# Performance work log

Measured on AMD Instinct MI355X. Metric: run time of the kernel, lower is better.

## Reference

```python
import jax, jax.numpy as jnp
import numpy as np

D_MODEL = 96
D_STATE = 6
D_CONV = 9
D_INNER = 2 * D_MODEL          # expand = 2
DT_RANK = (D_MODEL + 15) // 16  # ceil(d_model/16) = 6
DIM_IN = 64
DIM_OUT = 64
BATCH = 16
SEQLEN = 4096


def setup_inputs() -> dict:
    key = jax.random.key(0)
    ks = jax.random.split(key, 12)
    def s(k, shape, scale=0.02):
        return jax.random.normal(k, shape, jnp.float32) * scale
    return {
        "x": jax.random.normal(ks[0], (BATCH, SEQLEN, D_MODEL), jnp.float32),
        # Mamba block params
        "in_proj_w": s(ks[1], (2 * D_INNER, D_MODEL)),
        "conv_w": s(ks[2], (D_INNER, D_CONV), 0.1),   # depthwise conv kernel
        "conv_b": jnp.zeros((D_INNER,), jnp.float32),
        "x_proj_w": s(ks[3], (DT_RANK + 2 * D_STATE, D_INNER)),
        "dt_proj_w": s(ks[4], (D_INNER, DT_RANK), 0.1),
        "dt_proj_b": s(ks[5], (D_INNER,), 0.1),
        "A_log": jnp.log(jnp.tile(jnp.arange(1, D_STATE + 1, dtype=jnp.float32), (D_INNER, 1))),
        "D_param": jnp.ones((D_INNER,), jnp.float32),
        "out_proj_w": s(ks[6], (D_MODEL, D_INNER)),
        "norm_w": jnp.ones((D_MODEL,), jnp.float32),  # RMSNorm weight
        # heads
        "out_fc_w": s(ks[7], (DIM_IN, D_MODEL)),
        "out_fc_b": jnp.zeros((DIM_IN,), jnp.float32),
        "mu_w": s(ks[8], (DIM_OUT, DIM_IN)),
        "mu_b": jnp.zeros((DIM_OUT,), jnp.float32),
        "sigma_w": s(ks[9], (DIM_OUT, DIM_IN)),
        "sigma_b": jnp.zeros((DIM_OUT,), jnp.float32),
    }


def _mamba_block(x, in_proj_w, conv_w, conv_b, x_proj_w, dt_proj_w, dt_proj_b,
                 A_log, D_param, out_proj_w):
    Bsz = x.shape[0]
    xz = jnp.einsum('bld,ed->ble', x, in_proj_w)          # (B,L,2*ED)
    xs, z = jnp.split(xz, 2, axis=-1)
    # causal depthwise conv1d (torch pads d_conv-1 both sides then trims right)
    xt = xs.transpose(0, 2, 1)                            # (B,ED,L)
    kern = conv_w[:, None, :]                             # (ED,1,K)
    xc = jax.lax.conv_general_dilated(xt, kern, window_strides=(1,),
                                      padding=[(D_CONV - 1, 0)],
                                      feature_group_count=D_INNER)
    xc = (xc + conv_b[None, :, None]).transpose(0, 2, 1)  # (B,L,ED)
    xc = jax.nn.silu(xc)
    dbc = jnp.einsum('ble,fe->blf', xc, x_proj_w)         # (B,L,dt_rank+2N)
    delta_r = dbc[..., :DT_RANK]
    Bm = dbc[..., DT_RANK:DT_RANK + D_STATE]              # (B,L,N)
    Cm = dbc[..., DT_RANK + D_STATE:]                     # (B,L,N)
    delta = jax.nn.softplus(jnp.einsum('blr,er->ble', delta_r, dt_proj_w) + dt_proj_b)
    A = -jnp.exp(A_log)                                   # (ED,N)
    deltaA = jnp.exp(delta[..., None] * A)                # (B,L,ED,N)
    BX = (delta * xc)[..., None] * Bm[:, :, None, :]      # (B,L,ED,N)

    def step(h, inputs):
        dA, bx = inputs
        h = dA * h + bx
        return h, h

    h0 = jnp.zeros((Bsz, D_INNER, D_STATE), x.dtype)
    _, hs = jax.lax.scan(step, h0, (deltaA.swapaxes(0, 1), BX.swapaxes(0, 1)))
    y = jnp.einsum('lben,bln->ble', hs, Cm)               # (B,L,ED)
    y = y + D_param * xc
    y = y * jax.nn.silu(z)
    return jnp.einsum('ble,de->bld', y, out_proj_w)       # (B,L,D)


def reference(x, in_proj_w, conv_w, conv_b, x_proj_w, dt_proj_w, dt_proj_b,
              A_log, D_param, out_proj_w, norm_w,
              out_fc_w, out_fc_b, mu_w, mu_b, sigma_w, sigma_b):
    # residual block: x + mixer(RMSNorm(x))   (dropout is identity at eval)
    h = x * jax.lax.rsqrt(jnp.mean(x * x, axis=-1, keepdims=True) + 1e-5) * norm_w
    out = x + _mamba_block(h, in_proj_w, conv_w, conv_b, x_proj_w,
                           dt_proj_w, dt_proj_b, A_log, D_param, out_proj_w)
    e = out.mean(axis=1)                                  # (B,D)
    feat = jax.nn.elu(jnp.tanh(e @ out_fc_w.T + out_fc_b))
    mu = feat @ mu_w.T + mu_b
    sigma = jax.nn.elu(feat @ sigma_w.T + sigma_b) + 1.0 + 1e-14
    return (feat, mu, sigma)
```

## Files before the change

### kernel.cpp

```cpp
#include <hip/hip_runtime.h>
#include <math.h>

#define BATCH 16
#define SEQLEN 4096
#define D_MODEL 96
#define D_STATE 6
#define D_CONV 9
#define D_INNER 192
#define DT_RANK 6
#define NPOS (BATCH * SEQLEN)

#define NC2 128
#define CT2 (SEQLEN / NC2)
#define NSEG 16
#define CPS (NC2 / NSEG)

#define OFF_XS    0L
#define OFF_Z     (OFF_XS   + (long)NPOS * 96)
#define OFF_OUT4  (OFF_Z    + (long)NPOS * 96)
#define OFF_SEG   (OFF_OUT4 + (long)BATCH * NC2 * 5 * 192 * 4)
#define OFF_XPART (OFF_SEG  + (long)BATCH * NSEG * 5 * 192 * 4)

typedef short v8s __attribute__((ext_vector_type(8)));
typedef float v4f __attribute__((ext_vector_type(4)));

__device__ __forceinline__ float silu_fast(float v) {
    return __fdividef(v, 1.0f + __expf(-v));
}
__device__ __forceinline__ float softplus_fast(float v) {
    return (v > 20.0f) ? v : __logf(1.0f + __expf(v));
}
__device__ __forceinline__ float eluf(float v) {
    return (v > 0.0f) ? v : expm1f(v);
}
__device__ __forceinline__ unsigned int pack_bf16(float a, float b) {
    unsigned int ua = __float_as_uint(a), ub = __float_as_uint(b);
    ua += 0x7FFFu + ((ua >> 16) & 1u);
    ub += 0x7FFFu + ((ub >> 16) & 1u);
    return (ua >> 16) | (ub & 0xFFFF0000u);
}
__device__ __forceinline__ unsigned short bf16h(float v) {
    unsigned int u = __float_as_uint(v);
    u += 0x7FFFu + ((u >> 16) & 1u);
    return (unsigned short)(u >> 16);
}
__device__ __forceinline__ float bf2f(unsigned short h) {
    return __uint_as_float(((unsigned int)h) << 16);
}

#define TP1 64
__global__ __launch_bounds__(256, 2) void k1_rmsnorm_inproj(
    const float* __restrict__ x, const float* __restrict__ W,
    const float* __restrict__ norm_w,
    unsigned short* __restrict__ xs, unsigned short* __restrict__ z,
    float* __restrict__ xpart)
{
    __shared__ unsigned int s_ovl[7680];
    __shared__ unsigned int s_hA[64 * 52];
    __shared__ float s_part[TP1][4];
    __shared__ float s_scale[TP1];
    float* hRow = (float*)s_ovl;
    unsigned int* WB = s_ovl;

    const int tid = threadIdx.x;
    const long p0 = (long)blockIdx.x * TP1;

    {
        const float4* x4 = (const float4*)&x[p0 * 96];
        for (int i = tid; i < TP1 * 24; i += 256) {
            int p = i / 24, dq = i - p * 24;
            float4 v = x4[i];
            float* hr = &hRow[p * 101 + dq * 4];
            hr[0] = v.x; hr[1] = v.y; hr[2] = v.z; hr[3] = v.w;
        }
    }
    __syncthreads();

    {
        int p = tid >> 2, g = tid & 3;
        float ss = 0.0f;
        for (int d = g; d < 96; d += 4) { float v = hRow[p * 101 + d]; ss += v * v; }
        s_part[p][g] = ss;
    }
    __syncthreads();

    if (tid < TP1) {
        float ss = s_part[tid][0] + s_part[tid][1] + s_part[tid][2] + s_part[tid][3];
        s_scale[tid] = 1.0f / sqrtf(ss / 96.0f + 1e-5f);
    } else if (tid < TP1 + 96) {
        int d = tid - TP1;
        float s = 0.0f;
        for (int p = 0; p < TP1; p++) s += hRow[p * 101 + d];
        xpart[(long)blockIdx.x * 96 + d] = s;
    }
    __syncthreads();

    {
        const float2* nw2 = (const float2*)norm_w;
        for (int i = tid; i < TP1 * 48; i += 256) {
            int p = i / 48, dp = i - p * 48;
            float sc = s_scale[p];
            float2 nv = nw2[dp];
            float v0 = hRow[p * 101 + 2 * dp]     * sc * nv.x;
            float v1 = hRow[p * 101 + 2 * dp + 1] * sc * nv.y;
            s_hA[p * 52 + dp] = pack_bf16(v0, v1);
        }
    }
    __syncthreads();

    const int wave = tid >> 6, lane = tid & 63;
    const int quad = lane >> 4, ln = lane & 15;
    const int n0 = wave * 96;
    unsigned int* WBw = WB + wave * 1920;

    v4f acc[4][6];
#pragma unroll
    for (int mt = 0; mt < 4; mt++)
#pragma unroll
        for (int nt = 0; nt < 6; nt++) acc[mt][nt] = (v4f){0.f, 0.f, 0.f, 0.f};

    for (int kc = 0; kc < 3; kc++) {
#pragma unroll 8
        for (int ii = 0; ii < 24; ii++) {
            int i = lane + ii * 64;
            int jp = i >> 4, kp = i & 15;
            const float2 wv = *(const float2*)&W[(n0 + jp) * 96 + kc * 32 + 2 * kp];
            WBw[jp * 20 + kp] = pack_bf16(wv.x, wv.y);
        }
        v8s bfh[4];
#pragma unroll
        for (int mt = 0; mt < 4; mt++)
            bfh[mt] = *(const v8s*)&s_hA[(mt * 16 + ln) * 52 + kc * 16 + quad * 4];
#pragma unroll
        for (int nt = 0; nt < 6; nt++) {
            v8s aw = *(const v8s*)&WBw[(nt * 16 + ln) * 20 + quad * 4];
#pragma unroll
            for (int mt = 0; mt < 4; mt++)
                acc[mt][nt] = __builtin_amdgcn_mfma_f32_16x16x32_bf16(
                    aw, bfh[mt], acc[mt][nt], 0, 0, 0);
        }
    }

    unsigned short* dst = (wave < 2) ? xs : z;
    const int jb = (wave & 1) * 96;
#pragma unroll
    for (int mt = 0; mt < 4; mt++) {
        long pos = p0 + mt * 16 + ln;
#pragma unroll
        for (int nt = 0; nt < 6; nt++) {
            uint2 v;
            v.x = pack_bf16(acc[mt][nt][0], acc[mt][nt][1]);
            v.y = pack_bf16(acc[mt][nt][2], acc[mt][nt][3]);
            *(uint2*)&dst[pos * D_INNER + jb + nt * 16 + quad * 4] = v;
        }
    }
}

#define SXSTR 200
__global__ __launch_bounds__(192, 4) void k2f_conv_scan(
    const unsigned short* __restrict__ xs, const unsigned short* __restrict__ z,
    const float* __restrict__ conv_w, const float* __restrict__ conv_b,
    const float* __restrict__ x_proj_w,
    const float* __restrict__ dt_w, const float* __restrict__ dt_b,
    const float* __restrict__ A_log, const float* __restrict__ D_param,
    float4* __restrict__ out4)
{
    __shared__ unsigned short sxc[CT2 * SXSTR];
    __shared__ unsigned short sxpB[18 * SXSTR];
    __shared__ float sMeta[CT2][20];
    const int e = threadIdx.x;
    const int c = blockIdx.x & (NC2 - 1);
    const int b = blockIdx.x >> 7;
    const int l0 = c * CT2;
    const long brow = (long)b * SEQLEN;

    {
        unsigned int* xpB = (unsigned int*)sxpB;
        for (int i = e; i < 18 * 96; i += 192) {
            int f = i / 96, kp = i - f * 96;
            const float2 wv = *(const float2*)&x_proj_w[f * 192 + 2 * kp];
            xpB[f * 100 + kp] = pack_bf16(wv.x, wv.y);
        }
    }

    float cw[D_CONV];
#pragma unroll
    for (int k = 0; k < D_CONV; k++) cw[k] = conv_w[e * D_CONV + k];
    const float cb = conv_b[e];
    float win[D_CONV];
#pragma unroll
    for (int k = 0; k < 8; k++) {
        int ll = l0 - 8 + k;
        win[k] = (ll >= 0) ? bf2f(xs[(brow + ll) * D_INNER + e]) : 0.0f;
    }
#pragma unroll
    for (int r = 0; r < CT2; r++) {
        win[8] = bf2f(xs[(brow + l0 + r) * D_INNER + e]);
        float s = cb;
#pragma unroll
        for (int k = 0; k < D_CONV; k++) s += win[k] * cw[k];
        sxc[r * SXSTR + e] = bf16h(silu_fast(s));
#pragma unroll
        for (int k = 0; k < 8; k++) win[k] = win[k + 1];
    }

    const unsigned short* zp = &z[(brow + l0) * D_INNER + e];
    float zv[CT2];
#pragma unroll
    for (int t = 0; t < CT2; t++) zv[t] = bf2f(zp[(long)t * D_INNER]);
    __syncthreads();

    {
        const int wave = e >> 6, lane = e & 63;
        const int quad = lane >> 4, ln = lane & 15;
        if (wave < 2) {
            const int mt = wave;
            const int r1 = (ln < 2) ? 16 + ln : 0;
            v4f dacc[2];
            dacc[0] = (v4f){0.f, 0.f, 0.f, 0.f};
            dacc[1] = (v4f){0.f, 0.f, 0.f, 0.f};
#pragma unroll
            for (int kc = 0; kc < 6; kc++) {
                v8s af  = *(const v8s*)&sxc[(mt * 16 + ln) * SXSTR + kc * 32 + quad * 8];
                v8s bf0 = *(const v8s*)&sxpB[ln * SXSTR + kc * 32 + quad * 8];
                v8s bf1 = *(const v8s*)&sxpB[r1 * SXSTR + kc * 32 + quad * 8];
                dacc[0] = __builtin_amdgcn_mfma_f32_16x16x32_bf16(af, bf0, dacc[0], 0, 0, 0);
                dacc[1] = __builtin_amdgcn_mfma_f32_16x16x32_bf16(af, bf1, dacc[1], 0, 0, 0);
            }
#pragma unroll
            for (int nt = 0; nt < 2; nt++) {
                int f = nt * 16 + ln;
                if (f < 18) {
                    int col = (f < 6) ? f : f + 2;
#pragma unroll
                    for (int r = 0; r < 4; r++)
                        sMeta[mt * 16 + quad * 4 + r][col] = dacc[nt][r];
                }
            }
        }
    }
    __syncthreads();

    float a[D_STATE];
#pragma unroll
    for (int n = 0; n < D_STATE; n++) a[n] = -__expf(A_log[e * D_STATE + n]);
    float dtw[DT_RANK];
#pragma unroll
    for (int q = 0; q < DT_RANK; q++) dtw[q] = dt_w[e * DT_RANK + q];
    const float dtb = dt_b[e];
    const float Dv = D_param[e];
    const float a0 = a[0];

    bool pok = true;
#pragma unroll
    for (int n = 1; n < D_STATE; n++)
        pok = pok && (fabsf(a[n] - (float)(n + 1) * a0)
                      <= 1e-4f * (float)(n + 1) * fabsf(a0));
    unsigned long long pmask = __ballot(pok);

    float S[D_STATE], G[D_STATE];
#pragma unroll
    for (int n = 0; n < D_STATE; n++) { S[n] = 0.0f; G[n] = 0.0f; }
    float ysum0 = 0.0f;

    if (pmask == 0xFFFFFFFFFFFFFFFFull) {
        float Pa = 1.0f;
#pragma unroll 2
        for (int t = 0; t < CT2; t++) {
            const float4* m4 = (const float4*)&sMeta[t][0];
            float4 m0 = m4[0], m1 = m4[1], mB0 = m4[2], mB1 = m4[3], mC = m4[4];
            float Bv[6] = {mB0.x, mB0.y, mB0.z, mB0.w, mB1.x, mB1.y};
            float Cv[6] = {mB1.z, mB1.w, mC.x, mC.y, mC.z, mC.w};
            float dr = dtb + m0.x * dtw[0] + m0.y * dtw[1] + m0.z * dtw[2]
                     + m0.w * dtw[3] + m1.x * dtw[4] + m1.y * dtw[5];
            float dl = softplus_fast(dr);
            float xv = bf2f(sxc[t * SXSTR + e]);
            float zw = silu_fast(zv[t]);
            float dx = dl * xv;
            float y = Dv * xv;
            float E = __expf(dl * a0);
            Pa *= E;
            float dA = E, Pn = Pa;
#pragma unroll
            for (int n = 0; n < D_STATE; n++) {
                S[n] = dA * S[n] + dx * Bv[n];
                y += S[n] * Cv[n];
                G[n] += zw * Pn * Cv[n];
                dA *= E;
                Pn *= Pa;
            }
            ysum0 += zw * y;
        }
        long ob = (long)(b * NC2 + c) * 5 * 192 + e;
        float P1 = Pa, P2 = P1 * Pa, P3 = P2 * Pa, P4 = P3 * Pa, P5 = P4 * Pa, P6 = P5 * Pa;
        float4 q0, q1, q2, q3, q4;
        q0.x=P1; q0.y=P2; q0.z=P3; q0.w=P4;
        q1.x=P5; q1.y=P6; q1.z=S[0]; q1.w=S[1];
        q2.x=S[2]; q2.y=S[3]; q2.z=S[4]; q2.w=S[5];
        q3.x=G[0]; q3.y=G[1]; q3.z=G[2]; q3.w=G[3];
        q4.x=G[4]; q4.y=G[5]; q4.z=ysum0; q4.w=0.0f;
        out4[ob          ] = q0;
        out4[ob + 192    ] = q1;
        out4[ob + 2 * 192] = q2;
        out4[ob + 3 * 192] = q3;
        out4[ob + 4 * 192] = q4;
    } else {
        float P[D_STATE];
#pragma unroll
        for (int n = 0; n < D_STATE; n++) P[n] = 1.0f;
#pragma unroll 2
        for (int t = 0; t < CT2; t++) {
            const float4* m4 = (const float4*)&sMeta[t][0];
            float4 m0 = m4[0], m1 = m4[1], mB0 = m4[2], mB1 = m4[3], mC = m4[4];
            float Bv[6] = {mB0.x, mB0.y, mB0.z, mB0.w, mB1.x, mB1.y};
            float Cv[6] = {mB1.z, mB1.w, mC.x, mC.y, mC.z, mC.w};
            float dr = dtb + m0.x * dtw[0] + m0.y * dtw[1] + m0.z * dtw[2]
                     + m0.w * dtw[3] + m1.x * dtw[4] + m1.y * dtw[5];
            float dl = softplus_fast(dr);
            float xv = bf2f(sxc[t * SXSTR + e]);
            float zw = silu_fast(zv[t]);
            float dx = dl * xv;
            float y = Dv * xv;
#pragma unroll
            for (int n = 0; n < D_STATE; n++) {
                float dA = __expf(dl * a[n]);
                S[n] = dA * S[n] + dx * Bv[n];
                P[n] *= dA;
                y += S[n] * Cv[n];
                G[n] += zw * P[n] * Cv[n];
            }
            ysum0 += zw * y;
        }
        long ob = (long)(b * NC2 + c) * 5 * 192 + e;
        float4 q0, q1, q2, q3, q4;
        q0.x=P[0]; q0.y=P[1]; q0.z=P[2]; q0.w=P[3];
        q1.x=P[4]; q1.y=P[5]; q1.z=S[0]; q1.w=S[1];
        q2.x=S[2]; q2.y=S[3]; q2.z=S[4]; q2.w=S[5];
        q3.x=G[0]; q3.y=G[1]; q3.z=G[2]; q3.w=G[3];
        q4.x=G[4]; q4.y=G[5]; q4.z=ysum0; q4.w=0.0f;
        out4[ob          ] = q0;
        out4[ob + 192    ] = q1;
        out4[ob + 2 * 192] = q2;
        out4[ob + 3 * 192] = q3;
        out4[ob + 4 * 192] = q4;
    }
}

__global__ __launch_bounds__(192) void k4_seg(
    const float4* __restrict__ out4, float4* __restrict__ seg4)
{
    const int e = threadIdx.x;
    const int s = blockIdx.x & (NSEG - 1);
    const int b = blockIdx.x >> 4;

    float H[D_STATE], Gq[D_STATE], Pp[D_STATE];
#pragma unroll
    for (int n = 0; n < D_STATE; n++) { H[n] = 0.0f; Gq[n] = 0.0f; Pp[n] = 1.0f; }
    float yb = 0.0f;
#pragma unroll 2
    for (int cc = 0; cc < CPS; cc++) {
        int c = s * CPS + cc;
        long ob = (long)(b * NC2 + c) * 5 * 192 + e;
        float4 q0 = out4[ob];
        float4 q1 = out4[ob + 192];
        float4 q2 = out4[ob + 2 * 192];
        float4 q3 = out4[ob + 3 * 192];
        float4 q4 = out4[ob + 4 * 192];
        float Pv[6] = {q0.x, q0.y, q0.z, q0.w, q1.x, q1.y};
        float Sv[6] = {q1.z, q1.w, q2.x, q2.y, q2.z, q2.w};
        float Gv[6] = {q3.x, q3.y, q3.z, q3.w, q4.x, q4.y};
        float g = 0.0f;
#pragma unroll
        for (int n = 0; n < D_STATE; n++) g += Gv[n] * H[n];
        yb += q4.z + g;
#pragma unroll
        for (int n = 0; n < D_STATE; n++) {
            Gq[n] += Gv[n] * Pp[n];
            H[n] = Pv[n] * H[n] + Sv[n];
            Pp[n] *= Pv[n];
        }
    }
    long sb = (long)(b * NSEG + s) * 5 * 192 + e;
    float4 q0, q1, q2, q3, q4;
    q0.x=Pp[0]; q0.y=Pp[1]; q0.z=Pp[2]; q0.w=Pp[3];
    q1.x=Pp[4]; q1.y=Pp[5]; q1.z=H[0]; q1.w=H[1];
    q2.x=H[2]; q2.y=H[3]; q2.z=H[4]; q2.w=H[5];
    q3.x=Gq[0]; q3.y=Gq[1]; q3.z=Gq[2]; q3.w=Gq[3];
    q4.x=Gq[4]; q4.y=Gq[5]; q4.z=yb; q4.w=0.0f;
    seg4[sb          ] = q0;
    seg4[sb + 192    ] = q1;
    seg4[sb + 2 * 192] = q2;
    seg4[sb + 3 * 192] = q3;
    seg4[sb + 4 * 192] = q4;
}

__global__ __launch_bounds__(192) void k4_head(
    const float4* __restrict__ seg4, const float* __restrict__ xpart,
    const float* __restrict__ Wout,
    const float* __restrict__ fc_w, const float* __restrict__ fc_b,
    const float* __restrict__ mu_w, const float* __restrict__ mu_b,
    const float* __restrict__ sg_w, const float* __restrict__ sg_b,
    float* __restrict__ out)
{
    __shared__ float ybar[D_INNER];
    __shared__ float sxb[D_MODEL];
    __shared__ float evec[D_MODEL];
    __shared__ float feat_s[64];
    const int e = threadIdx.x;
    const int b = blockIdx.x;

    float H[D_STATE];
#pragma unroll
    for (int n = 0; n < D_STATE; n++) H[n] = 0.0f;
    float yb = 0.0f;
#pragma unroll 4
    for (int s = 0; s < NSEG; s++) {
        long ob = (long)(b * NSEG + s) * 5 * 192 + e;
        float4 q0 = seg4[ob];
        float4 q1 = seg4[ob + 192];
        float4 q2 = seg4[ob + 2 * 192];
        float4 q3 = seg4[ob + 3 * 192];
        float4 q4 = seg4[ob + 4 * 192];
        float Pv[6] = {q0.x, q0.y, q0.z, q0.w, q1.x, q1.y};
        float Sv[6] = {q1.z, q1.w, q2.x, q2.y, q2.z, q2.w};
        float Gv[6] = {q3.x, q3.y, q3.z, q3.w, q4.x, q4.y};
        float g = 0.0f;
#pragma unroll
        for (int n = 0; n < D_STATE; n++) g += Gv[n] * H[n];
        yb += q4.z + g;
#pragma unroll
        for (int n = 0; n < D_STATE; n++) H[n] = Pv[n] * H[n] + Sv[n];
    }
    ybar[e] = yb;

    if (e < D_MODEL) {
        const float* xp = &xpart[(long)b * 64 * 96 + e];
        float s = 0.0f;
        for (int t = 0; t < 64; t++) s += xp[t * 96];
        sxb[e] = s;
    }
    __syncthreads();

    if (e < D_MODEL) {
        float s = sxb[e];
        const float* wrow = &Wout[e * D_INNER];
        for (int e2 = 0; e2 < D_INNER; e2++) s += ybar[e2] * wrow[e2];
        evec[e] = s / (float)SEQLEN;
    }
    __syncthreads();

    if (e < 64) {
        float s = fc_b[e];
        const float* wrow = &fc_w[e * D_MODEL];
        for (int d = 0; d < D_MODEL; d++) s += evec[d] * wrow[d];
        float f = eluf(tanhf(s));
        feat_s[e] = f;
        out[b * 64 + e] = f;
    }
    __syncthreads();

    if (e < 64) {
        float smu = mu_b[e], ssg = sg_b[e];
        const float* mrow = &mu_w[e * 64];
        const float* srow = &sg_w[e * 64];
        for (int i = 0; i < 64; i++) {
            smu += feat_s[i] * mrow[i];
            ssg += feat_s[i] * srow[i];
        }
        out[1024 + b * 64 + e] = smu;
        out[2048 + b * 64 + e] = eluf(ssg) + 1.0f + 1e-14f;
    }
}

extern "C" void kernel_launch(void* const* d_in, const int* in_sizes, int n_in,
                              void* d_out, int out_size, void* d_ws, size_t ws_size,
                              hipStream_t stream) {
    const float* x         = (const float*)d_in[0];
    const float* in_proj_w = (const float*)d_in[1];
    const float* conv_w    = (const float*)d_in[2];
    const float* conv_b    = (const float*)d_in[3];
    const float* x_proj_w  = (const float*)d_in[4];
    const float* dt_proj_w = (const float*)d_in[5];
    const float* dt_proj_b = (const float*)d_in[6];
    const float* A_log     = (const float*)d_in[7];
    const float* D_param   = (const float*)d_in[8];
    const float* out_proj_w= (const float*)d_in[9];
    const float* norm_w    = (const float*)d_in[10];
    const float* out_fc_w  = (const float*)d_in[11];
    const float* out_fc_b  = (const float*)d_in[12];
    const float* mu_w      = (const float*)d_in[13];
    const float* mu_b      = (const float*)d_in[14];
    const float* sigma_w   = (const float*)d_in[15];
    const float* sigma_b   = (const float*)d_in[16];
    float* ws = (float*)d_ws;
    float* out = (float*)d_out;

    k1_rmsnorm_inproj<<<NPOS / TP1, 256, 0, stream>>>(
        x, in_proj_w, norm_w,
        (unsigned short*)(ws + OFF_XS), (unsigned short*)(ws + OFF_Z),
        ws + OFF_XPART);

    k2f_conv_scan<<<BATCH * NC2, 192, 0, stream>>>(
        (const unsigned short*)(ws + OFF_XS), (const unsigned short*)(ws + OFF_Z),
        conv_w, conv_b, x_proj_w,
        dt_proj_w, dt_proj_b, A_log, D_param,
        (float4*)(ws + OFF_OUT4));

    k4_seg<<<BATCH * NSEG, 192, 0, stream>>>(
        (const float4*)(ws + OFF_OUT4), (float4*)(ws + OFF_SEG));

    k4_head<<<BATCH, 192, 0, stream>>>(
        (const float4*)(ws + OFF_SEG), ws + OFF_XPART, out_proj_w,
        out_fc_w, out_fc_b, mu_w, mu_b, sigma_w, sigma_b, out);
}
```

Baseline: 202.1 us.

## Halve scan chunk count to 64 per batch, doubling chunk length

The conv+scan kernel now uses 64 chunks of 64 timesteps instead of 128 chunks of 32. This halves the number of blocks and per-chunk summaries written and later combined, and each chunk's MFMA x_proj now covers four 16-row tiles. The z values are loaded in two 32-step batches to keep register pressure bounded. Fewer blocks (1024) means less parallelism and a longer serial recurrence per thread, and shared memory per block doubles, which may lower occupancy.

```diff
diff --git a/kernel.cpp b/kernel.cpp
--- a/kernel.cpp
+++ b/kernel.cpp
@@ -10,7 +10,7 @@
 #define DT_RANK 6
 #define NPOS (BATCH * SEQLEN)
 
-#define NC2 128
+#define NC2 64
 #define CT2 (SEQLEN / NC2)
 #define NSEG 16
 #define CPS (NC2 / NSEG)
@@ -170,7 +170,7 @@
     __shared__ float sMeta[CT2][20];
     const int e = threadIdx.x;
     const int c = blockIdx.x & (NC2 - 1);
-    const int b = blockIdx.x >> 7;
+    const int b = blockIdx.x >> 6;
     const int l0 = c * CT2;
     const long brow = (long)b * SEQLEN;
 
@@ -203,38 +203,36 @@
 #pragma unroll
         for (int k = 0; k < 8; k++) win[k] = win[k + 1];
     }
-
-    const unsigned short* zp = &z[(brow + l0) * D_INNER + e];
-    float zv[CT2];
-#pragma unroll
-    for (int t = 0; t < CT2; t++) zv[t] = bf2f(zp[(long)t * D_INNER]);
     __syncthreads();
 
     {
         const int wave = e >> 6, lane = e & 63;
         const int quad = lane >> 4, ln = lane & 15;
         if (wave < 2) {
-            const int mt = wave;
             const int r1 = (ln < 2) ? 16 + ln : 0;
-            v4f dacc[2];
-            dacc[0] = (v4f){0.f, 0.f, 0.f, 0.f};
-            dacc[1] = (v4f){0.f, 0.f, 0.f, 0.f};
-#pragma unroll
-            for (int kc = 0; kc < 6; kc++) {
-                v8s af  = *(const v8s*)&sxc[(mt * 16 + ln) * SXSTR + kc * 32 + quad * 8];
-                v8s bf0 = *(const v8s*)&sxpB[ln * SXSTR + kc * 32 + quad * 8];
-                v8s bf1 = *(const v8s*)&sxpB[r1 * SXSTR + kc * 32 + quad * 8];
-                dacc[0] = __builtin_amdgcn_mfma_f32_16x16x32_bf16(af, bf0, dacc[0], 0, 0, 0);
-                dacc[1] = __builtin_amdgcn_mfma_f32_16x16x32_bf16(af, bf1, dacc[1], 0, 0, 0);
-            }
-#pragma unroll
-            for (int nt = 0; nt < 2; nt++) {
-                int f = nt * 16 + ln;
-                if (f < 18) {
-                    int col = (f < 6) ? f : f + 2;
-#pragma unroll
-                    for (int r = 0; r < 4; r++)
-                        sMeta[mt * 16 + quad * 4 + r][col] = dacc[nt][r];
+#pragma unroll
+            for (int half = 0; half < 2; half++) {
+                const int mt = wave * 2 + half;
+                v4f dacc[2];
+                dacc[0] = (v4f){0.f, 0.f, 0.f, 0.f};
+                dacc[1] = (v4f){0.f, 0.f, 0.f, 0.f};
+#pragma unroll
+                for (int kc = 0; kc < 6; kc++) {
+                    v8s af  = *(const v8s*)&sxc[(mt * 16 + ln) * SXSTR + kc * 32 + quad * 8];
+                    v8s bf0 = *(const v8s*)&sxpB[ln * SXSTR + kc * 32 + quad * 8];
+                    v8s bf1 = *(const v8s*)&sxpB[r1 * SXSTR + kc * 32 + quad * 8];
+                    dacc[0] = __builtin_amdgcn_mfma_f32_16x16x32_bf16(af, bf0, dacc[0], 0, 0, 0);
+                    dacc[1] = __builtin_amdgcn_mfma_f32_16x16x32_bf16(af, bf1, dacc[1], 0, 0, 0);
+                }
+#pragma unroll
+                for (int nt = 0; nt < 2; nt++) {
+                    int f = nt * 16 + ln;
+                    if (f < 18) {
+                        int col = (f < 6) ? f : f + 2;
+#pragma unroll
+                        for (int r = 0; r < 4; r++)
+                            sMeta[mt * 16 + quad * 4 + r][col] = dacc[nt][r];
+                    }
                 }
             }
         }
@@ -262,34 +260,41 @@
 #pragma unroll
     for (int n = 0; n < D_STATE; n++) { S[n] = 0.0f; G[n] = 0.0f; }
     float ysum0 = 0.0f;
+    float zvb[32];
 
     if (pmask == 0xFFFFFFFFFFFFFFFFull) {
         float Pa = 1.0f;
+        for (int tb = 0; tb < 2; tb++) {
+            const unsigned short* zp = &z[(brow + l0 + tb * 32) * D_INNER + e];
+#pragma unroll
+            for (int t = 0; t < 32; t++) zvb[t] = bf2f(zp[(long)t * D_INNER]);
 #pragma unroll 2
-        for (int t = 0; t < CT2; t++) {
-            const float4* m4 = (const float4*)&sMeta[t][0];
-            float4 m0 = m4[0], m1 = m4[1], mB0 = m4[2], mB1 = m4[3], mC = m4[4];
-            float Bv[6] = {mB0.x, mB0.y, mB0.z, mB0.w, mB1.x, mB1.y};
-            float Cv[6] = {mB1.z, mB1.w, mC.x, mC.y, mC.z, mC.w};
-            float dr = dtb + m0.x * dtw[0] + m0.y * dtw[1] + m0.z * dtw[2]
-                     + m0.w * dtw[3] + m1.x * dtw[4] + m1.y * dtw[5];
-            float dl = softplus_fast(dr);
-            float xv = bf2f(sxc[t * SXSTR + e]);
-            float zw = silu_fast(zv[t]);
-            float dx = dl * xv;
-            float y = Dv * xv;
-            float E = __expf(dl * a0);
-            Pa *= E;
-            float dA = E, Pn = Pa;
-#pragma unroll
-            for (int n = 0; n < D_STATE; n++) {
-                S[n] = dA * S[n] + dx * Bv[n];
-                y += S[n] * Cv[n];
-                G[n] += zw * Pn * Cv[n];
-                dA *= E;
-                Pn *= Pa;
+            for (int tt = 0; tt < 32; tt++) {
+                const int t = tb * 32 + tt;
+                const float4* m4 = (const float4*)&sMeta[t][0];
+                float4 m0 = m4[0], m1 = m4[1], mB0 = m4[2], mB1 = m4[3], mC = m4[4];
+                float Bv[6] = {mB0.x, mB0.y, mB0.z, mB0.w, mB1.x, mB1.y};
+                float Cv[6] = {mB1.z, mB1.w, mC.x, mC.y, mC.z, mC.w};
+                float dr = dtb + m0.x * dtw[0] + m0.y * dtw[1] + m0.z * dtw[2]
+                         + m0.w * dtw[3] + m1.x * dtw[4] + m1.y * dtw[5];
+                float dl = softplus_fast(dr);
+                float xv = bf2f(sxc[t * SXSTR + e]);
+                float zw = silu_fast(zvb[tt]);
+                float dx = dl * xv;
+                float y = Dv * xv;
+                float E = __expf(dl * a0);
+                Pa *= E;
+                float dA = E, Pn = Pa;
+#pragma unroll
+                for (int n = 0; n < D_STATE; n++) {
+                    S[n] = dA * S[n] + dx * Bv[n];
+                    y += S[n] * Cv[n];
+                    G[n] += zw * Pn * Cv[n];
+                    dA *= E;
+                    Pn *= Pa;
+                }
+                ysum0 += zw * y;
             }
-            ysum0 += zw * y;
         }
         long ob = (long)(b * NC2 + c) * 5 * 192 + e;
         float P1 = Pa, P2 = P1 * Pa, P3 = P2 * Pa, P4 = P3 * Pa, P5 = P4 * Pa, P6 = P5 * Pa;
@@ -308,28 +313,34 @@
         float P[D_STATE];
 #pragma unroll
         for (int n = 0; n < D_STATE; n++) P[n] = 1.0f;
+        for (int tb = 0; tb < 2; tb++) {
+            const unsigned short* zp = &z[(brow + l0 + tb * 32) * D_INNER + e];
+#pragma unroll
+            for (int t = 0; t < 32; t++) zvb[t] = bf2f(zp[(long)t * D_INNER]);
 #pragma unroll 2
-        for (int t = 0; t < CT2; t++) {
-            const float4* m4 = (const float4*)&sMeta[t][0];
-            float4 m0 = m4[0], m1 = m4[1], mB0 = m4[2], mB1 = m4[3], mC = m4[4];
-            float Bv[6] = {mB0.x, mB0.y, mB0.z, mB0.w, mB1.x, mB1.y};
-            float Cv[6] = {mB1.z, mB1.w, mC.x, mC.y, mC.z, mC.w};
-            float dr = dtb + m0.x * dtw[0] + m0.y * dtw[1] + m0.z * dtw[2]
-                     + m0.w * dtw[3] + m1.x * dtw[4] + m1.y * dtw[5];
-            float dl = softplus_fast(dr);
-            float xv = bf2f(sxc[t * SXSTR + e]);
-            float zw = silu_fast(zv[t]);
-            float dx = dl * xv;
-            float y = Dv * xv;
-#pragma unroll
-            for (int n = 0; n < D_STATE; n++) {
-                float dA = __expf(dl * a[n]);
-                S[n] = dA * S[n] + dx * Bv[n];
-                P[n] *= dA;
-                y += S[n] * Cv[n];
-                G[n] += zw * P[n] * Cv[n];
+            for (int tt = 0; tt < 32; tt++) {
+                const int t = tb * 32 + tt;
+                const float4* m4 = (const float4*)&sMeta[t][0];
+                float4 m0 = m4[0], m1 = m4[1], mB0 = m4[2], mB1 = m4[3], mC = m4[4];
+                float Bv[6] = {mB0.x, mB0.y, mB0.z, mB0.w, mB1.x, mB1.y};
+                float Cv[6] = {mB1.z, mB1.w, mC.x, mC.y, mC.z, mC.w};
+                float dr = dtb + m0.x * dtw[0] + m0.y * dtw[1] + m0.z * dtw[2]
+                         + m0.w * dtw[3] + m1.x * dtw[4] + m1.y * dtw[5];
+                float dl = softplus_fast(dr);
+                float xv = bf2f(sxc[t * SXSTR + e]);
+                float zw = silu_fast(zvb[tt]);
+                float dx = dl * xv;
+                float y = Dv * xv;
+#pragma unroll
+                for (int n = 0; n < D_STATE; n++) {
+                    float dA = __expf(dl * a[n]);
+                    S[n] = dA * S[n] + dx * Bv[n];
+                    P[n] *= dA;
+                    y += S[n] * Cv[n];
+                    G[n] += zw * P[n] * Cv[n];
+                }
+                ysum0 += zw * y;
             }
-            ysum0 += zw * y;
         }
         long ob = (long)(b * NC2 + c) * 5 * 192 + e;
         float4 q0, q1, q2, q3, q4;
@@ -357,7 +368,7 @@
 #pragma unroll
     for (int n = 0; n < D_STATE; n++) { H[n] = 0.0f; Gq[n] = 0.0f; Pp[n] = 1.0f; }
     float yb = 0.0f;
-#pragma unroll 2
+#pragma unroll
     for (int cc = 0; cc < CPS; cc++) {
         int c = s * CPS + cc;
         long ob = (long)(b * NC2 + c) * 5 * 192 + e;
```

After: 213.6 us. 5.7% more time.
